# Optimization experiments

Measured on AMD Instinct MI355X. Metric: run time of the kernel, lower is better.

## Reference

```python
import jax, jax.numpy as jnp
import numpy as np

# --- Mamba2Simple hyperparams (from module defaults + headdim=64 hardcode) ---
D_MODEL = 512
D_STATE = 128
EXPAND = 2
HEADDIM = 64
D_INNER = EXPAND * D_MODEL          # 1024
NHEADS = D_INNER // HEADDIM         # 16
NGROUPS = 1
D_CONV = 4
CHUNK = 128                          # SSD chunk length
CONV_DIM = D_INNER + 2 * NGROUPS * D_STATE          # 1280
D_IN_PROJ = 2 * D_INNER + 2 * NGROUPS * D_STATE + NHEADS  # 2320
B_SZ, SEQ = 4, 4096
EPS = 1e-5


def setup_inputs() -> dict:
    key = jax.random.key(0)
    ks = jax.random.split(key, 8)
    x = jax.random.normal(ks[0], (B_SZ, SEQ, D_MODEL), jnp.float32)
    W_in = jax.random.normal(ks[1], (D_IN_PROJ, D_MODEL), jnp.float32) * 0.02
    conv_w = jax.random.normal(ks[2], (CONV_DIM, D_CONV), jnp.float32) * 0.1
    conv_b = jnp.zeros((CONV_DIM,), jnp.float32)
    # dt_bias = inverse-softplus of dt in [1e-3, 0.1] (mamba2 init)
    dt = jax.random.uniform(ks[3], (NHEADS,), jnp.float32, 1e-3, 0.1)
    dt_bias = jnp.log(jnp.expm1(dt))
    A_log = jnp.log(jax.random.uniform(ks[4], (NHEADS,), jnp.float32, 1.0, 16.0))
    D = jnp.ones((NHEADS,), jnp.float32)
    norm_w = jnp.ones((D_INNER,), jnp.float32)
    W_out = jax.random.normal(ks[5], (D_MODEL, D_INNER), jnp.float32) * 0.02
    return dict(x=x, W_in=W_in, conv_w=conv_w, conv_b=conv_b, dt_bias=dt_bias,
                A_log=A_log, D=D, norm_w=norm_w, W_out=W_out)


def _causal_conv(x, w, b):
    """Depthwise causal conv1d. x: (b,l,c), w: (c,K), b: (c,)."""
    lhs = x.transpose(0, 2, 1)          # (b,c,l)
    rhs = w[:, None, :]                  # (c,1,K) depthwise
    out = jax.lax.conv_general_dilated(lhs, rhs, (1,), [(D_CONV - 1, 0)],
                                       feature_group_count=CONV_DIM)
    return out.transpose(0, 2, 1) + b


def _segsum(a):
    """a: (..., T) -> (..., T, T) with out[i,j] = sum_{j<k<=i} a[k], -inf above diag."""
    T = a.shape[-1]
    cs = jnp.cumsum(a, -1)
    seg = cs[..., :, None] - cs[..., None, :]
    mask = jnp.tril(jnp.ones((T, T), bool))
    return jnp.where(mask, seg, -jnp.inf)


def _ssd(X, A, B, C):
    """Chunked SSD scan (ssd_minimal_discrete).
    X: (b,l,h,p) (= dt*x), A: (b,l,h) (= dt*A, negative), B,C: (b,l,n). ngroups=1.
    """
    b, l, h, p = X.shape
    c = l // CHUNK
    Xc = X.reshape(b, c, CHUNK, h, p)
    Ac = A.reshape(b, c, CHUNK, h).transpose(0, 3, 1, 2)   # (b,h,c,q)
    Bc = B.reshape(b, c, CHUNK, -1)                         # (b,c,q,n)
    Cc = C.reshape(b, c, CHUNK, -1)
    A_cs = jnp.cumsum(Ac, -1)                               # (b,h,c,q)
    # intra-chunk (quadratic) part
    Lmat = jnp.exp(_segsum(Ac))                             # (b,h,c,q,q) causal decay
    Y_diag = jnp.einsum('bcqn,bcsn,bhcqs,bcshp->bcqhp', Cc, Bc, Lmat, Xc)
    # per-chunk final states
    decay_states = jnp.exp(A_cs[..., -1:] - A_cs)           # (b,h,c,q)
    states = jnp.einsum('bcqn,bhcq,bcqhp->bchpn', Bc, decay_states, Xc)
    # inter-chunk recurrence (initial state = 0)
    A_last = jnp.pad(A_cs[..., -1], ((0, 0), (0, 0), (1, 0)))  # (b,h,c+1)
    decay_chunk = jnp.exp(_segsum(A_last))                     # (b,h,c+1,c+1)
    states = jnp.concatenate([jnp.zeros_like(states[:, :1]), states], axis=1)
    new_states = jnp.einsum('bhzc,bchpn->bzhpn', decay_chunk, states)
    prev_states = new_states[:, :-1]                           # (b,c,h,p,n)
    Y_off = jnp.einsum('bcqn,bchpn,bhcq->bcqhp', Cc, prev_states, jnp.exp(A_cs))
    return (Y_diag + Y_off).reshape(b, l, h, p)


def _forward(x, W_in, conv_w, conv_b, dt_bias, A_log, D, norm_w, W_out):
    bsz, L, _ = x.shape
    zxbcdt = x @ W_in.T                                   # (b,l,2320)
    z = zxbcdt[..., :D_INNER]
    xBC = zxbcdt[..., D_INNER:D_INNER + CONV_DIM]
    dt = jax.nn.softplus(zxbcdt[..., -NHEADS:] + dt_bias)  # (b,l,h)
    xBC = jax.nn.silu(_causal_conv(xBC, conv_w, conv_b))
    xs = xBC[..., :D_INNER].reshape(bsz, L, NHEADS, HEADDIM)
    Bm = xBC[..., D_INNER:D_INNER + D_STATE]               # (b,l,n)
    Cm = xBC[..., D_INNER + D_STATE:]                      # (b,l,n)
    A = -jnp.exp(A_log)                                    # (h,)
    y = _ssd(xs * dt[..., None], dt * A, Bm, Cm)           # (b,l,h,p)
    y = y + D[None, None, :, None] * xs                    # D skip
    y = y.reshape(bsz, L, D_INNER)
    # gated RMSNorm (norm_before_gate=False): rmsnorm(y * silu(z)) * w
    g = y * jax.nn.silu(z)
    g = g * jax.lax.rsqrt(jnp.mean(g * g, -1, keepdims=True) + EPS) * norm_w
    return x + g @ W_out.T                                 # residual add


def reference(x, W_in, conv_w, conv_b, dt_bias, A_log, D, norm_w, W_out):
    return _forward(x, W_in, conv_w, conv_b, dt_bias, A_log, D, norm_w, W_out)
```

## Files before the change

kernel.cpp:

```cpp
#include <hip/hip_runtime.h>
#include <hip/hip_bf16.h>

typedef __hip_bfloat16 bf16;
typedef __attribute__((ext_vector_type(8))) __bf16 bf16x8;
typedef __attribute__((ext_vector_type(4))) float f32x4;

constexpr int BSZ = 4, SEQ = 4096, DMODEL = 512;
constexpr int DSTATE = 128, HEADDIM = 64, DINNER = 1024, NHEADS = 16, CHUNK = 128;
constexpr int CONVDIM = DINNER + 2 * DSTATE;
constexpr int DINPROJ = 2 * DINNER + 2 * DSTATE + NHEADS;
constexpr int NPAD = 2432;
constexpr int MTOT = BSZ * SEQ;
constexpr int NCHUNK = SEQ / CHUNK;

constexpr size_t OFF_Z    = 0;
constexpr size_t OFF_XBC  = OFF_Z    + (size_t)MTOT * DINNER * 2;
constexpr size_t OFF_DT   = OFF_XBC  + (size_t)MTOT * CONVDIM * 2;
constexpr size_t OFF_XS   = OFF_DT   + (size_t)MTOT * NHEADS * 4;
constexpr size_t OFF_B    = OFF_XS   + (size_t)MTOT * DINNER * 2;
constexpr size_t OFF_C    = OFF_B    + (size_t)MTOT * DSTATE * 2;
constexpr size_t OFF_G    = OFF_C    + (size_t)MTOT * DSTATE * 2;
constexpr size_t OFF_ASUM = OFF_G    + (size_t)BSZ * NCHUNK * CHUNK * CHUNK * 2;
constexpr size_t WS_NEED  = OFF_ASUM + 8192;

static __device__ __forceinline__ float sigmoidf_(float x) { return 1.f / (1.f + __expf(-x)); }
static __device__ __forceinline__ unsigned short f2bf_bits(float f) {
    __hip_bfloat16 h = __float2bfloat16(f);
    return *reinterpret_cast<unsigned short*>(&h);
}
static __device__ __forceinline__ float bfbits2f(unsigned short u) {
    return __bfloat162float(*reinterpret_cast<bf16*>(&u));
}
struct us4 { unsigned short a, b, c, d; };
static __device__ __forceinline__ us4 pack4(const f32x4 v) {
    return { f2bf_bits(v[0]), f2bf_bits(v[1]), f2bf_bits(v[2]), f2bf_bits(v[3]) };
}

__global__ void k_sentinel(float* out) { out[0] = 1.0e9f; }

__global__ __launch_bounds__(256) void k_cast_x(const float* __restrict__ in, bf16* __restrict__ out, int n4) {
    int i = blockIdx.x * 256 + threadIdx.x;
    if (i >= n4) return;
    float4 f = ((const float4*)in)[i];
    us4 v = { f2bf_bits(f.x), f2bf_bits(f.y), f2bf_bits(f.z), f2bf_bits(f.w) };
    ((us4*)out)[i] = v;
}

__global__ __launch_bounds__(256) void k_cast_win(const float* __restrict__ W, bf16* __restrict__ out) {
    int i = blockIdx.x * 256 + threadIdx.x;
    if (i >= NPAD * (DMODEL / 4)) return;
    int row = i / (DMODEL / 4);
    us4 v;
    if (row < DINPROJ) {
        float4 f = ((const float4*)W)[i];
        v = { f2bf_bits(f.x), f2bf_bits(f.y), f2bf_bits(f.z), f2bf_bits(f.w) };
    } else {
        v = { 0, 0, 0, 0 };
    }
    ((us4*)out)[i] = v;
}

typedef const __attribute__((address_space(1))) void* gas_t;
typedef __attribute__((address_space(3))) void* las_t;
static __device__ __forceinline__ void gload_lds16(const void* g, void* l) {
    __builtin_amdgcn_global_load_lds((gas_t)g, (las_t)l, 16, 0, 0);
}

template<int K>
static __device__ __forceinline__ void gemm_core(
    const bf16* __restrict__ A, const bf16* __restrict__ B,
    int m0, int n0, bf16* ldsA, bf16* ldsB, f32x4 acc[4][4])
{
    constexpr int NT = K / 32;
    const int tid = threadIdx.x;
    const int l = tid & 63, w = tid >> 6;
    const int wr = w >> 1, wc = w & 1;
    const int lq = l & 15, lk = l >> 4;

    auto stage = [&](int buf, int t) {
        const int k0 = t * 32;
        #pragma unroll
        for (int i = 0; i < 2; ++i) {
            int q = w * 16 + i * 8 + (l >> 3);
            int p = l & 7;
            int L = p ^ (q & 7);
            int ra = (L >> 2) * 64 + q;
            int ck = L & 3;
            gload_lds16(A + (size_t)(m0 + ra) * K + k0 + ck * 8,
                        ldsA + buf * 4096 + (w * 16 + i * 8) * 64);
            gload_lds16(B + (size_t)(n0 + ra) * K + k0 + ck * 8,
                        ldsB + buf * 4096 + (w * 16 + i * 8) * 64);
        }
    };

    stage(0, 0);
    stage(1, 1);
    for (int t = 0; t < NT; ++t) {
        if (t + 1 < NT) asm volatile("s_waitcnt vmcnt(4)" ::: "memory");
        else            asm volatile("s_waitcnt vmcnt(0)" ::: "memory");
        __builtin_amdgcn_s_barrier();
        __builtin_amdgcn_sched_barrier(0);
        if (t + 2 < NT) stage((t + 2) % 3, t + 2);
        const int buf = t % 3;
        bf16x8 av[4], bv[4];
        #pragma unroll
        for (int f = 0; f < 4; ++f) {
            int ra = wr * 64 + f * 16 + lq;
            int qa = ra & 63, La = (ra >> 6) * 4 + lk, pa = La ^ (qa & 7);
            av[f] = *(const bf16x8*)(ldsA + buf * 4096 + qa * 64 + pa * 8);
            int rb = wc * 64 + f * 16 + lq;
            int qb = rb & 63, Lb = (rb >> 6) * 4 + lk, pb = Lb ^ (qb & 7);
            bv[f] = *(const bf16x8*)(ldsB + buf * 4096 + qb * 64 + pb * 8);
        }
        #pragma unroll
        for (int nf = 0; nf < 4; ++nf)
            #pragma unroll
            for (int mf = 0; mf < 4; ++mf)
                acc[nf][mf] = __builtin_amdgcn_mfma_f32_16x16x32_bf16(bv[nf], av[mf], acc[nf][mf], 0, 0, 0);
    }
}

static __device__ __forceinline__ void swz_block(int& bx, int& by) {
    int gx = gridDim.x;
    int nwg = gx * gridDim.y;
    int wg = by * gx + bx;
    int q = nwg >> 3;
    wg = (wg & 7) * q + (wg >> 3);
    bx = wg % gx; by = wg / gx;
}

__global__ __launch_bounds__(256) void k_gemm_in(
    const bf16* __restrict__ xb, const bf16* __restrict__ Wb,
    const float* __restrict__ dt_bias,
    bf16* __restrict__ z, bf16* __restrict__ xbc, float* __restrict__ dtb)
{
    __shared__ bf16 ldsA[3 * 4096];
    __shared__ bf16 ldsB[3 * 4096];
    int bx = blockIdx.x, by = blockIdx.y;
    swz_block(bx, by);
    const int m0 = by * 128, n0 = bx * 128;
    f32x4 acc[4][4] = {};
    gemm_core<DMODEL>(xb, Wb, m0, n0, ldsA, ldsB, acc);
    const int l = threadIdx.x & 63, w = threadIdx.x >> 6;
    const int wr = w >> 1, wc = w & 1, lq = l & 15, lk = l >> 4;
    const int mg = m0 + wr * 64, ng = n0 + wc * 64;
    if (n0 < DINNER) {
        #pragma unroll
        for (int nf = 0; nf < 4; ++nf)
            #pragma unroll
            for (int mf = 0; mf < 4; ++mf) {
                int n = ng + nf * 16 + lk * 4;
                int m = mg + mf * 16 + lq;
                *(us4*)(z + (size_t)m * DINNER + n) = pack4(acc[nf][mf]);
            }
    } else if (n0 < DINNER + CONVDIM) {
        #pragma unroll
        for (int nf = 0; nf < 4; ++nf)
            #pragma unroll
            for (int mf = 0; mf < 4; ++mf) {
                int n = ng + nf * 16 + lk * 4 - DINNER;
                int m = mg + mf * 16 + lq;
                *(us4*)(xbc + (size_t)m * CONVDIM + n) = pack4(acc[nf][mf]);
            }
    } else {
        #pragma unroll
        for (int nf = 0; nf < 4; ++nf)
            #pragma unroll
            for (int mf = 0; mf < 4; ++mf)
                #pragma unroll
                for (int j = 0; j < 4; ++j) {
                    int n = ng + nf * 16 + lk * 4 + j;
                    int m = mg + mf * 16 + lq;
                    if (n < DINPROJ) {
                        int h = n - (DINNER + CONVDIM);
                        float t = acc[nf][mf][j] + dt_bias[h];
                        dtb[(size_t)m * NHEADS + h] = (t > 20.f) ? t : log1pf(__expf(t));
                    }
                }
    }
}

__global__ __launch_bounds__(256) void k_gemm_out(
    const bf16* __restrict__ gb, const bf16* __restrict__ Wb,
    const float* __restrict__ xres, float* __restrict__ outp)
{
    __shared__ bf16 ldsA[3 * 4096];
    __shared__ bf16 ldsB[3 * 4096];
    int bx = blockIdx.x, by = blockIdx.y;
    swz_block(bx, by);
    const int m0 = by * 128, n0 = bx * 128;
    f32x4 acc[4][4] = {};
    gemm_core<DINNER>(gb, Wb, m0, n0, ldsA, ldsB, acc);
    const int l = threadIdx.x & 63, w = threadIdx.x >> 6;
    const int wr = w >> 1, wc = w & 1, lq = l & 15, lk = l >> 4;
    const int mg = m0 + wr * 64, ng = n0 + wc * 64;
    #pragma unroll
    for (int nf = 0; nf < 4; ++nf)
        #pragma unroll
        for (int mf = 0; mf < 4; ++mf) {
            int n = ng + nf * 16 + lk * 4;
            int m = mg + mf * 16 + lq;
            float4 r = *(const float4*)(xres + (size_t)m * DMODEL + n);
            float4 o = { r.x + acc[nf][mf][0], r.y + acc[nf][mf][1],
                         r.z + acc[nf][mf][2], r.w + acc[nf][mf][3] };
            *(float4*)(outp + (size_t)m * DMODEL + n) = o;
        }
}

constexpr int CTOK = 8;
__global__ __launch_bounds__(320) void k_conv(
    const bf16* __restrict__ xbc, const float* __restrict__ cw, const float* __restrict__ cb,
    bf16* __restrict__ xs, bf16* __restrict__ Bm, bf16* __restrict__ Cm)
{
    const int m0 = blockIdx.x * CTOK;
    const int c4 = threadIdx.x;
    const int c = c4 * 4;
    const int l0 = m0 & 4095;
    float4 cbv = ((const float4*)cb)[c4];
    const float4 w0 = ((const float4*)cw)[c + 0];
    const float4 w1 = ((const float4*)cw)[c + 1];
    const float4 w2 = ((const float4*)cw)[c + 2];
    const float4 w3 = ((const float4*)cw)[c + 3];
    us4 rows[CTOK + 3];
    #pragma unroll
    for (int t = -3; t < CTOK; ++t) {
        int ll = l0 + t;
        if (ll >= 0) rows[t + 3] = *(const us4*)(xbc + (size_t)(m0 + t) * CONVDIM + c);
        else         rows[t + 3] = { 0, 0, 0, 0 };
    }
    #pragma unroll
    for (int t = 0; t < CTOK; ++t) {
        float a0 = cbv.x, a1 = cbv.y, a2 = cbv.z, a3 = cbv.w;
        #pragma unroll
        for (int k = 0; k < 4; ++k) {
            us4 v = rows[t + k];
            a0 += bfbits2f(v.a) * ((const float*)&w0)[k];
            a1 += bfbits2f(v.b) * ((const float*)&w1)[k];
            a2 += bfbits2f(v.c) * ((const float*)&w2)[k];
            a3 += bfbits2f(v.d) * ((const float*)&w3)[k];
        }
        us4 o = { f2bf_bits(a0 * sigmoidf_(a0)), f2bf_bits(a1 * sigmoidf_(a1)),
                  f2bf_bits(a2 * sigmoidf_(a2)), f2bf_bits(a3 * sigmoidf_(a3)) };
        int m = m0 + t;
        if (c < DINNER)               *(us4*)(xs + (size_t)m * DINNER + c) = o;
        else if (c < DINNER + DSTATE) *(us4*)(Bm + (size_t)m * DSTATE + (c - DINNER)) = o;
        else                          *(us4*)(Cm + (size_t)m * DSTATE + (c - DINNER - DSTATE)) = o;
    }
}

__global__ __launch_bounds__(64) void k_gmat(
    const bf16* __restrict__ Cm, const bf16* __restrict__ Bm, bf16* __restrict__ G)
{
    const int bc = blockIdx.z;
    const int q0 = blockIdx.x * 64, s0 = blockIdx.y * 64;
    const int row0 = bc * CHUNK;
    const int l = threadIdx.x;
    const int lq = l & 15, lk = l >> 4;
    f32x4 acc[4][4] = {};
    #pragma unroll
    for (int kc = 0; kc < 4; ++kc) {
        bf16x8 av[4], bv[4];
        #pragma unroll
        for (int f = 0; f < 4; ++f) {
            av[f] = *(const bf16x8*)(Cm + (size_t)(row0 + q0 + f * 16 + lq) * DSTATE + kc * 32 + lk * 8);
            bv[f] = *(const bf16x8*)(Bm + (size_t)(row0 + s0 + f * 16 + lq) * DSTATE + kc * 32 + lk * 8);
        }
        #pragma unroll
        for (int fs = 0; fs < 4; ++fs)
            #pragma unroll
            for (int fq = 0; fq < 4; ++fq)
                acc[fs][fq] = __builtin_amdgcn_mfma_f32_16x16x32_bf16(bv[fs], av[fq], acc[fs][fq], 0, 0, 0);
    }
    #pragma unroll
    for (int fs = 0; fs < 4; ++fs)
        #pragma unroll
        for (int fq = 0; fq < 4; ++fq) {
            int q = q0 + fq * 16 + lq;
            int s = s0 + fs * 16 + lk * 4;
            *(us4*)(G + ((size_t)bc * CHUNK + q) * CHUNK + s) = pack4(acc[fs][fq]);
        }
}

__global__ __launch_bounds__(256) void k_ssd(
    const bf16* __restrict__ xs , const bf16* __restrict__ Bm,
    const float* __restrict__ dtb, const float* __restrict__ A_log,
    const float* __restrict__ Dp, const bf16* __restrict__ G,
    bf16* __restrict__ y, bf16* __restrict__ states, float* __restrict__ asum)
{
    const int h = blockIdx.x, c = blockIdx.y, b = blockIdx.z;
    const int tid = threadIdx.x;
    const int l = tid & 63, w = tid >> 6;
    const int lq = l & 15, lk = l >> 4;
    __shared__ float sa[CHUNK], sdt[CHUNK], sdec[CHUNK];
    __shared__ __bf16 Xt[HEADDIM][136];
    __shared__ __bf16 Bt[DSTATE][136];
    const int row0 = b * SEQ + c * CHUNK;
    const int bc = b * NCHUNK + c;
    const float Ah = -__expf(A_log[h]);
    const float Dh = Dp[h];
    if (tid < CHUNK) {
        float d = dtb[(size_t)(row0 + tid) * NHEADS + h];
        sdt[tid] = d;
        sa[tid] = d * Ah;
    }
    __syncthreads();
    for (int off = 1; off < CHUNK; off <<= 1) {
        float v = 0.f;
        if (tid < CHUNK && tid >= off) v = sa[tid - off];
        __syncthreads();
        if (tid < CHUNK) sa[tid] += v;
        __syncthreads();
    }
    const float alast = sa[CHUNK - 1];
    if (tid < CHUNK) sdec[tid] = __expf(alast - sa[tid]);
    __syncthreads();
    {
        const int s = tid >> 1;
        const float dts = sdt[s];
        #pragma unroll
        for (int li = 0; li < 4; ++li) {
            int p0 = (tid & 1) * 8 + li * 16;
            bf16x8 v = *(const bf16x8*)(xs + (size_t)(row0 + s) * DINNER + h * HEADDIM + p0);
            #pragma unroll
            for (int i = 0; i < 8; ++i) Xt[p0 + i][s] = (__bf16)((float)v[i] * dts);
        }
        #pragma unroll
        for (int li = 0; li < 8; ++li) {
            int n0 = (tid & 1) * 8 + li * 16;
            bf16x8 v = *(const bf16x8*)(Bm + (size_t)(row0 + s) * DSTATE + n0);
            #pragma unroll
            for (int i = 0; i < 8; ++i) Bt[n0 + i][s] = v[i];
        }
    }
    __syncthreads();
    {
        const int q0 = w * 32;
        f32x4 acc[4][2] = {};
        #pragma unroll
        for (int kc = 0; kc < 4; ++kc) {
            const int sbase = kc * 32 + lk * 8;
            bf16x8 av[2];
            #pragma unroll
            for (int fr = 0; fr < 2; ++fr) {
                int q = q0 + fr * 16 + lq;
                bf16x8 g = *(const bf16x8*)(G + ((size_t)bc * CHUNK + q) * CHUNK + sbase);
                float saq = sa[q];
                bf16x8 wv;
                #pragma unroll
                for (int j = 0; j < 8; ++j) {
                    int s = sbase + j;
                    float val = (s <= q) ? __expf(saq - sa[s]) * (float)g[j] : 0.f;
                    wv[j] = (__bf16)val;
                }
                av[fr] = wv;
            }
            #pragma unroll
            for (int pf = 0; pf < 4; ++pf) {
                bf16x8 xv = *(const bf16x8*)&Xt[pf * 16 + lq][sbase];
                #pragma unroll
                for (int fr = 0; fr < 2; ++fr)
                    acc[pf][fr] = __builtin_amdgcn_mfma_f32_16x16x32_bf16(xv, av[fr], acc[pf][fr], 0, 0, 0);
            }
        }
        #pragma unroll
        for (int fr = 0; fr < 2; ++fr)
            #pragma unroll
            for (int pf = 0; pf < 4; ++pf) {
                int q = q0 + fr * 16 + lq;
                int p = pf * 16 + lk * 4;
                size_t idx = (size_t)(row0 + q) * DINNER + h * HEADDIM + p;
                us4 xv4 = *(const us4*)(xs + idx);
                f32x4 a = acc[pf][fr];
                us4 o = { f2bf_bits(a[0] + Dh * bfbits2f(xv4.a)),
                          f2bf_bits(a[1] + Dh * bfbits2f(xv4.b)),
                          f2bf_bits(a[2] + Dh * bfbits2f(xv4.c)),
                          f2bf_bits(a[3] + Dh * bfbits2f(xv4.d)) };
                *(us4*)(y + idx) = o;
            }
    }
    {
        const int n0 = w * 32;
        f32x4 acc[2][4] = {};
        #pragma unroll
        for (int kc = 0; kc < 4; ++kc) {
            const int sbase = kc * 32 + lk * 8;
            bf16x8 xd[4];
            #pragma unroll
            for (int pf = 0; pf < 4; ++pf) {
                bf16x8 xv = *(const bf16x8*)&Xt[pf * 16 + lq][sbase];
                bf16x8 sc;
                #pragma unroll
                for (int j = 0; j < 8; ++j) sc[j] = (__bf16)((float)xv[j] * sdec[sbase + j]);
                xd[pf] = sc;
            }
            #pragma unroll
            for (int nf = 0; nf < 2; ++nf) {
                bf16x8 bb = *(const bf16x8*)&Bt[n0 + nf * 16 + lq][sbase];
                #pragma unroll
                for (int pf = 0; pf < 4; ++pf)
                    acc[nf][pf] = __builtin_amdgcn_mfma_f32_16x16x32_bf16(bb, xd[pf], acc[nf][pf], 0, 0, 0);
            }
        }
        const size_t sb = ((size_t)bc * NHEADS + h) * (HEADDIM * DSTATE);
        #pragma unroll
        for (int nf = 0; nf < 2; ++nf)
            #pragma unroll
            for (int pf = 0; pf < 4; ++pf) {
                int p = pf * 16 + lq;
                int n = n0 + nf * 16 + lk * 4;
                *(us4*)(states + sb + (size_t)p * DSTATE + n) = pack4(acc[nf][pf]);
            }
    }
    if (tid == 0) asum[bc * NHEADS + h] = alast;
}

__global__ __launch_bounds__(256) void k_scan(bf16* __restrict__ states, const float* __restrict__ asum)
{
    const int h = blockIdx.x, b = blockIdx.y, seg = blockIdx.z;
    const int e0 = seg * 512 + threadIdx.x;
    float P[2];
    P[0] = 0.f; P[1] = 0.f;
    for (int c = 0; c < NCHUNK; ++c) {
        size_t base = ((size_t)(b * NCHUNK + c) * NHEADS + h) * (HEADDIM * DSTATE);
        float dec = __expf(asum[(b * NCHUNK + c) * NHEADS + h]);
        #pragma unroll
        for (int j = 0; j < 2; ++j) {
            size_t e = base + e0 + j * 256;
            float sc = __bfloat162float(states[e]);
            states[e] = __float2bfloat16(P[j]);
            P[j] = dec * P[j] + sc;
        }
    }
}

__global__ __launch_bounds__(256) void k_yoff(
    const bf16* __restrict__ Cm,
    const float* __restrict__ dtb, const float* __restrict__ A_log,
    const bf16* __restrict__ states,
    bf16* __restrict__ y)
{
    const int h = blockIdx.x, c = blockIdx.y, b = blockIdx.z;
    const int tid = threadIdx.x;
    const int l = tid & 63, w = tid >> 6;
    const int lq = l & 15, lk = l >> 4;
    __shared__ float sa[CHUNK];
    const int row0 = b * SEQ + c * CHUNK;
    const int bc = b * NCHUNK + c;
    const float Ah = -__expf(A_log[h]);
    if (tid < CHUNK) {
        float d = dtb[(size_t)(row0 + tid) * NHEADS + h];
        sa[tid] = d * Ah;
    }
    __syncthreads();
    for (int off = 1; off < CHUNK; off <<= 1) {
        float v = 0.f;
        if (tid < CHUNK && tid >= off) v = sa[tid - off];
        __syncthreads();
        if (tid < CHUNK) sa[tid] += v;
        __syncthreads();
    }
    const size_t sb = ((size_t)bc * NHEADS + h) * (HEADDIM * DSTATE);
    const int q0 = w * 32;
    f32x4 acc[4][2] = {};
    #pragma unroll
    for (int kc = 0; kc < 4; ++kc) {
        const int nbase = kc * 32 + lk * 8;
        bf16x8 av[2], bv[4];
        #pragma unroll
        for (int fr = 0; fr < 2; ++fr)
            av[fr] = *(const bf16x8*)(Cm + (size_t)(row0 + q0 + fr * 16 + lq) * DSTATE + nbase);
        #pragma unroll
        for (int fc = 0; fc < 4; ++fc)
            bv[fc] = *(const bf16x8*)(states + sb + (size_t)(fc * 16 + lq) * DSTATE + nbase);
        #pragma unroll
        for (int fc = 0; fc < 4; ++fc)
            #pragma unroll
            for (int fr = 0; fr < 2; ++fr)
                acc[fc][fr] = __builtin_amdgcn_mfma_f32_16x16x32_bf16(bv[fc], av[fr], acc[fc][fr], 0, 0, 0);
    }
    #pragma unroll
    for (int fr = 0; fr < 2; ++fr)
        #pragma unroll
        for (int fc = 0; fc < 4; ++fc) {
            int q = q0 + fr * 16 + lq;
            int p = fc * 16 + lk * 4;
            size_t idx = (size_t)(row0 + q) * DINNER + h * HEADDIM + p;
            const float eq = __expf(sa[q]);
            us4 cur = *(const us4*)(y + idx);
            f32x4 a = acc[fc][fr];
            us4 o = { f2bf_bits(bfbits2f(cur.a) + eq * a[0]),
                      f2bf_bits(bfbits2f(cur.b) + eq * a[1]),
                      f2bf_bits(bfbits2f(cur.c) + eq * a[2]),
                      f2bf_bits(bfbits2f(cur.d) + eq * a[3]) };
            *(us4*)(y + idx) = o;
        }
}

__global__ __launch_bounds__(256) void k_norm(
    const bf16* __restrict__ y, const bf16* __restrict__ z,
    const float* __restrict__ norm_w, bf16* __restrict__ g)
{
    const int tid = threadIdx.x;
    const int tk = tid >> 7;
    const int lane = tid & 127;
    const int m = blockIdx.x * 2 + tk;
    const int e0 = lane * 8;
    bf16x8 z8 = *(const bf16x8*)(z + (size_t)m * DINNER + e0);
    bf16x8 y8 = *(const bf16x8*)(y + (size_t)m * DINNER + e0);
    float gg[8];
    float ss = 0.f;
    #pragma unroll
    for (int i = 0; i < 8; ++i) {
        float zz = (float)z8[i];
        gg[i] = (float)y8[i] * (zz * sigmoidf_(zz));
        ss += gg[i] * gg[i];
    }
    #pragma unroll
    for (int o = 32; o > 0; o >>= 1) ss += __shfl_xor(ss, o, 64);
    __shared__ float red[4];
    if ((tid & 63) == 0) red[tid >> 6] = ss;
    __syncthreads();
    const float scale = rsqrtf((red[tk * 2] + red[tk * 2 + 1]) / DINNER + 1e-5f);
    const float4 nw0 = *(const float4*)(norm_w + e0);
    const float4 nw1 = *(const float4*)(norm_w + e0 + 4);
    bf16x8 o8;
    o8[0] = (__bf16)(gg[0] * scale * nw0.x);
    o8[1] = (__bf16)(gg[1] * scale * nw0.y);
    o8[2] = (__bf16)(gg[2] * scale * nw0.z);
    o8[3] = (__bf16)(gg[3] * scale * nw0.w);
    o8[4] = (__bf16)(gg[4] * scale * nw1.x);
    o8[5] = (__bf16)(gg[5] * scale * nw1.y);
    o8[6] = (__bf16)(gg[6] * scale * nw1.z);
    o8[7] = (__bf16)(gg[7] * scale * nw1.w);
    *(bf16x8*)(g + (size_t)m * DINNER + e0) = o8;
}

extern "C" void kernel_launch(void* const* d_in, const int* in_sizes, int n_in,
                              void* d_out, int out_size, void* d_ws, size_t ws_size,
                              hipStream_t stream) {
    const float* x       = (const float*)d_in[0];
    const float* W_in    = (const float*)d_in[1];
    const float* conv_w  = (const float*)d_in[2];
    const float* conv_b  = (const float*)d_in[3];
    const float* dt_bias = (const float*)d_in[4];
    const float* A_log   = (const float*)d_in[5];
    const float* Dp      = (const float*)d_in[6];
    const float* norm_w  = (const float*)d_in[7];
    const float* W_out   = (const float*)d_in[8];
    float* out = (float*)d_out;

    if (ws_size < WS_NEED) {
        k_sentinel<<<1, 1, 0, stream>>>(out);
        return;
    }

    char* ws = (char*)d_ws;
    bf16* z     = (bf16*)(ws + OFF_Z);
    bf16* gb    = (bf16*)(ws + OFF_Z);
    bf16* xbc   = (bf16*)(ws + OFF_XBC);
    bf16* st    = (bf16*)(ws + OFF_XBC);
    float* dtb  = (float*)(ws + OFF_DT);
    bf16* xs    = (bf16*)(ws + OFF_XS);
    bf16* yb    = (bf16*)(ws + OFF_XS);
    bf16* xb    = (bf16*)(ws + OFF_XS);
    bf16* Bm    = (bf16*)(ws + OFF_B);
    bf16* Wbin  = (bf16*)(ws + OFF_B);
    bf16* Cm    = (bf16*)(ws + OFF_C);
    bf16* G     = (bf16*)(ws + OFF_G);
    bf16* Wbout = (bf16*)(ws + OFF_G);
    float* asum = (float*)(ws + OFF_ASUM);

    k_cast_x<<<(MTOT * DMODEL / 4 + 255) / 256, 256, 0, stream>>>(x, xb, MTOT * DMODEL / 4);
    k_cast_win<<<(NPAD * DMODEL / 4 + 255) / 256, 256, 0, stream>>>(W_in, Wbin);
    k_gemm_in<<<dim3(NPAD / 128, MTOT / 128), 256, 0, stream>>>(xb, Wbin, dt_bias, z, xbc, dtb);
    k_conv<<<MTOT / CTOK, 320, 0, stream>>>(xbc, conv_w, conv_b, xs, Bm, Cm);
    k_gmat<<<dim3(2, 2, BSZ * NCHUNK), 64, 0, stream>>>(Cm, Bm, G);
    k_ssd<<<dim3(NHEADS, NCHUNK, BSZ), 256, 0, stream>>>(xs, Bm, dtb, A_log, Dp, G, yb, st, asum);
    k_cast_x<<<(DMODEL * DINNER / 4 + 255) / 256, 256, 0, stream>>>(W_out, Wbout, DMODEL * DINNER / 4);
    k_scan<<<dim3(NHEADS, BSZ, 16), 256, 0, stream>>>(st, asum);
    k_yoff<<<dim3(NHEADS, NCHUNK, BSZ), 256, 0, stream>>>(Cm, dtb, A_log, st, yb);
    k_norm<<<MTOT / 2, 256, 0, stream>>>(yb, z, norm_w, gb);
    k_gemm_out<<<dim3(DMODEL / 128, MTOT / 128), 256, 0, stream>>>(gb, Wbout, x, out);
}
```

Baseline: 264.8 us.

## Retile input and output projection GEMMs to 256x256 tiles with 512 threads

Result: slower. 303.4 us (+14.6%).

```diff
diff --git a/kernel.cpp b/kernel.cpp
--- a/kernel.cpp
+++ b/kernel.cpp
@@ -9,7 +9,7 @@
 constexpr int DSTATE = 128, HEADDIM = 64, DINNER = 1024, NHEADS = 16, CHUNK = 128;
 constexpr int CONVDIM = DINNER + 2 * DSTATE;
 constexpr int DINPROJ = 2 * DINNER + 2 * DSTATE + NHEADS;
-constexpr int NPAD = 2432;
+constexpr int NPAD = 2560;
 constexpr int MTOT = BSZ * SEQ;
 constexpr int NCHUNK = SEQ / CHUNK;
 
@@ -67,56 +67,62 @@
 }
 
 template<int K>
-static __device__ __forceinline__ void gemm_core(
+static __device__ __forceinline__ void gemm256_core(
     const bf16* __restrict__ A, const bf16* __restrict__ B,
-    int m0, int n0, bf16* ldsA, bf16* ldsB, f32x4 acc[4][4])
+    int m0, int n0, bf16* ldsA, bf16* ldsB, f32x4 acc[8][4])
 {
     constexpr int NT = K / 32;
     const int tid = threadIdx.x;
     const int l = tid & 63, w = tid >> 6;
-    const int wr = w >> 1, wc = w & 1;
+    const int wr = w >> 2, wc = w & 3;
     const int lq = l & 15, lk = l >> 4;
 
     auto stage = [&](int buf, int t) {
         const int k0 = t * 32;
         #pragma unroll
         for (int i = 0; i < 2; ++i) {
-            int q = w * 16 + i * 8 + (l >> 3);
-            int p = l & 7;
+            int q = i * 64 + (tid >> 3);
+            int p = tid & 7;
             int L = p ^ (q & 7);
-            int ra = (L >> 2) * 64 + q;
+            int ra = (L >> 2) * 128 + q;
             int ck = L & 3;
             gload_lds16(A + (size_t)(m0 + ra) * K + k0 + ck * 8,
-                        ldsA + buf * 4096 + (w * 16 + i * 8) * 64);
+                        ldsA + buf * 8192 + i * 4096 + tid * 8);
             gload_lds16(B + (size_t)(n0 + ra) * K + k0 + ck * 8,
-                        ldsB + buf * 4096 + (w * 16 + i * 8) * 64);
+                        ldsB + buf * 8192 + i * 4096 + tid * 8);
         }
     };
 
+    int buf = 0;
     stage(0, 0);
-    stage(1, 1);
+    __syncthreads();
     for (int t = 0; t < NT; ++t) {
-        if (t + 1 < NT) asm volatile("s_waitcnt vmcnt(4)" ::: "memory");
-        else            asm volatile("s_waitcnt vmcnt(0)" ::: "memory");
-        __builtin_amdgcn_s_barrier();
+        if (t + 1 < NT) stage(buf ^ 1, t + 1);
         __builtin_amdgcn_sched_barrier(0);
-        if (t + 2 < NT) stage((t + 2) % 3, t + 2);
-        const int buf = t % 3;
-        bf16x8 av[4], bv[4];
+        bf16x8 av[8], bv[4];
+        #pragma unroll
+        for (int f = 0; f < 8; ++f) {
+            int ra = wr * 128 + f * 16 + lq;
+            int L = ((ra >> 7) << 2) | lk;
+            int q = ra & 127;
+            int p = L ^ (q & 7);
+            av[f] = *(const bf16x8*)(ldsA + buf * 8192 + q * 64 + p * 8);
+        }
         #pragma unroll
         for (int f = 0; f < 4; ++f) {
-            int ra = wr * 64 + f * 16 + lq;
-            int qa = ra & 63, La = (ra >> 6) * 4 + lk, pa = La ^ (qa & 7);
-            av[f] = *(const bf16x8*)(ldsA + buf * 4096 + qa * 64 + pa * 8);
             int rb = wc * 64 + f * 16 + lq;
-            int qb = rb & 63, Lb = (rb >> 6) * 4 + lk, pb = Lb ^ (qb & 7);
-            bv[f] = *(const bf16x8*)(ldsB + buf * 4096 + qb * 64 + pb * 8);
-        }
-        #pragma unroll
-        for (int nf = 0; nf < 4; ++nf)
-            #pragma unroll
-            for (int mf = 0; mf < 4; ++mf)
-                acc[nf][mf] = __builtin_amdgcn_mfma_f32_16x16x32_bf16(bv[nf], av[mf], acc[nf][mf], 0, 0, 0);
+            int L = ((rb >> 7) << 2) | lk;
+            int q = rb & 127;
+            int p = L ^ (q & 7);
+            bv[f] = *(const bf16x8*)(ldsB + buf * 8192 + q * 64 + p * 8);
+        }
+        #pragma unroll
+        for (int mf = 0; mf < 8; ++mf)
+            #pragma unroll
+            for (int nf = 0; nf < 4; ++nf)
+                acc[mf][nf] = __builtin_amdgcn_mfma_f32_16x16x32_bf16(bv[nf], av[mf], acc[mf][nf], 0, 0, 0);
+        __syncthreads();
+        buf ^= 1;
     }
 }
 
@@ -129,80 +135,80 @@
     bx = wg % gx; by = wg / gx;
 }
 
-__global__ __launch_bounds__(256) void k_gemm_in(
+__global__ __launch_bounds__(512, 2) void k_gemm_in(
     const bf16* __restrict__ xb, const bf16* __restrict__ Wb,
     const float* __restrict__ dt_bias,
     bf16* __restrict__ z, bf16* __restrict__ xbc, float* __restrict__ dtb)
 {
-    __shared__ bf16 ldsA[3 * 4096];
-    __shared__ bf16 ldsB[3 * 4096];
+    __shared__ bf16 ldsA[2 * 8192];
+    __shared__ bf16 ldsB[2 * 8192];
     int bx = blockIdx.x, by = blockIdx.y;
     swz_block(bx, by);
-    const int m0 = by * 128, n0 = bx * 128;
-    f32x4 acc[4][4] = {};
-    gemm_core<DMODEL>(xb, Wb, m0, n0, ldsA, ldsB, acc);
+    const int m0 = by * 256, n0 = bx * 256;
+    f32x4 acc[8][4] = {};
+    gemm256_core<DMODEL>(xb, Wb, m0, n0, ldsA, ldsB, acc);
     const int l = threadIdx.x & 63, w = threadIdx.x >> 6;
-    const int wr = w >> 1, wc = w & 1, lq = l & 15, lk = l >> 4;
-    const int mg = m0 + wr * 64, ng = n0 + wc * 64;
+    const int wr = w >> 2, wc = w & 3, lq = l & 15, lk = l >> 4;
+    const int mg = m0 + wr * 128, ng = n0 + wc * 64;
     if (n0 < DINNER) {
         #pragma unroll
-        for (int nf = 0; nf < 4; ++nf)
-            #pragma unroll
-            for (int mf = 0; mf < 4; ++mf) {
+        for (int mf = 0; mf < 8; ++mf)
+            #pragma unroll
+            for (int nf = 0; nf < 4; ++nf) {
                 int n = ng + nf * 16 + lk * 4;
                 int m = mg + mf * 16 + lq;
-                *(us4*)(z + (size_t)m * DINNER + n) = pack4(acc[nf][mf]);
+                *(us4*)(z + (size_t)m * DINNER + n) = pack4(acc[mf][nf]);
             }
     } else if (n0 < DINNER + CONVDIM) {
         #pragma unroll
-        for (int nf = 0; nf < 4; ++nf)
-            #pragma unroll
-            for (int mf = 0; mf < 4; ++mf) {
+        for (int mf = 0; mf < 8; ++mf)
+            #pragma unroll
+            for (int nf = 0; nf < 4; ++nf) {
                 int n = ng + nf * 16 + lk * 4 - DINNER;
                 int m = mg + mf * 16 + lq;
-                *(us4*)(xbc + (size_t)m * CONVDIM + n) = pack4(acc[nf][mf]);
+                *(us4*)(xbc + (size_t)m * CONVDIM + n) = pack4(acc[mf][nf]);
             }
     } else {
         #pragma unroll
-        for (int nf = 0; nf < 4; ++nf)
-            #pragma unroll
-            for (int mf = 0; mf < 4; ++mf)
+        for (int mf = 0; mf < 8; ++mf)
+            #pragma unroll
+            for (int nf = 0; nf < 4; ++nf)
                 #pragma unroll
                 for (int j = 0; j < 4; ++j) {
                     int n = ng + nf * 16 + lk * 4 + j;
                     int m = mg + mf * 16 + lq;
                     if (n < DINPROJ) {
                         int h = n - (DINNER + CONVDIM);
-                        float t = acc[nf][mf][j] + dt_bias[h];
+                        float t = acc[mf][nf][j] + dt_bias[h];
                         dtb[(size_t)m * NHEADS + h] = (t > 20.f) ? t : log1pf(__expf(t));
                     }
                 }
     }
 }
 
-__global__ __launch_bounds__(256) void k_gemm_out(
+__global__ __launch_bounds__(512, 2) void k_gemm_out(
     const bf16* __restrict__ gb, const bf16* __restrict__ Wb,
     const float* __restrict__ xres, float* __restrict__ outp)
 {
-    __shared__ bf16 ldsA[3 * 4096];
-    __shared__ bf16 ldsB[3 * 4096];
+    __shared__ bf16 ldsA[2 * 8192];
+    __shared__ bf16 ldsB[2 * 8192];
     int bx = blockIdx.x, by = blockIdx.y;
     swz_block(bx, by);
-    const int m0 = by * 128, n0 = bx * 128;
-    f32x4 acc[4][4] = {};
-    gemm_core<DINNER>(gb, Wb, m0, n0, ldsA, ldsB, acc);
+    const int m0 = by * 256, n0 = bx * 256;
+    f32x4 acc[8][4] = {};
+    gemm256_core<DINNER>(gb, Wb, m0, n0, ldsA, ldsB, acc);
     const int l = threadIdx.x & 63, w = threadIdx.x >> 6;
-    const int wr = w >> 1, wc = w & 1, lq = l & 15, lk = l >> 4;
-    const int mg = m0 + wr * 64, ng = n0 + wc * 64;
-    #pragma unroll
-    for (int nf = 0; nf < 4; ++nf)
-        #pragma unroll
-        for (int mf = 0; mf < 4; ++mf) {
+    const int wr = w >> 2, wc = w & 3, lq = l & 15, lk = l >> 4;
+    const int mg = m0 + wr * 128, ng = n0 + wc * 64;
+    #pragma unroll
+    for (int mf = 0; mf < 8; ++mf)
+        #pragma unroll
+        for (int nf = 0; nf < 4; ++nf) {
             int n = ng + nf * 16 + lk * 4;
             int m = mg + mf * 16 + lq;
             float4 r = *(const float4*)(xres + (size_t)m * DMODEL + n);
-            float4 o = { r.x + acc[nf][mf][0], r.y + acc[nf][mf][1],
-                         r.z + acc[nf][mf][2], r.w + acc[nf][mf][3] };
+            float4 o = { r.x + acc[mf][nf][0], r.y + acc[mf][nf][1],
+                         r.z + acc[mf][nf][2], r.w + acc[mf][nf][3] };
             *(float4*)(outp + (size_t)m * DMODEL + n) = o;
         }
 }
@@ -572,7 +578,7 @@
 
     k_cast_x<<<(MTOT * DMODEL / 4 + 255) / 256, 256, 0, stream>>>(x, xb, MTOT * DMODEL / 4);
     k_cast_win<<<(NPAD * DMODEL / 4 + 255) / 256, 256, 0, stream>>>(W_in, Wbin);
-    k_gemm_in<<<dim3(NPAD / 128, MTOT / 128), 256, 0, stream>>>(xb, Wbin, dt_bias, z, xbc, dtb);
+    k_gemm_in<<<dim3(NPAD / 256, MTOT / 256), 512, 0, stream>>>(xb, Wbin, dt_bias, z, xbc, dtb);
     k_conv<<<MTOT / CTOK, 320, 0, stream>>>(xbc, conv_w, conv_b, xs, Bm, Cm);
     k_gmat<<<dim3(2, 2, BSZ * NCHUNK), 64, 0, stream>>>(Cm, Bm, G);
     k_ssd<<<dim3(NHEADS, NCHUNK, BSZ), 256, 0, stream>>>(xs, Bm, dtb, A_log, Dp, G, yb, st, asum);
@@ -580,5 +586,5 @@
     k_scan<<<dim3(NHEADS, BSZ, 16), 256, 0, stream>>>(st, asum);
     k_yoff<<<dim3(NHEADS, NCHUNK, BSZ), 256, 0, stream>>>(Cm, dtb, A_log, st, yb);
     k_norm<<<MTOT / 2, 256, 0, stream>>>(yb, z, norm_w, gb);
-    k_gemm_out<<<dim3(DMODEL / 128, MTOT / 128), 256, 0, stream>>>(gb, Wbout, x, out);
-}
+    k_gemm_out<<<dim3(DMODEL / 256, MTOT / 256), 512, 0, stream>>>(gb, Wbout, x, out);
+}
```
